# Kernel tuning notes

Measured on AMD Instinct MI355X. Metric: run time of the kernel, lower is better.

## Reference

```python
import jax, jax.numpy as jnp
import numpy as np

B, L, S, D = 32, 256, 4, 512
H = L * S  # history_capacity
TGB = 128
VOCAB = 50000
LN_EPS = 1e-5


def _layer_norm(x, gamma, beta):
    mu = jnp.mean(x, axis=-1, keepdims=True)
    var = jnp.var(x, axis=-1, keepdims=True)
    return (x - mu) * jax.lax.rsqrt(var + LN_EPS) * gamma + beta


def setup_inputs() -> dict:
    key = jax.random.key(0)
    ks = jax.random.split(key, 16)
    inp = {
        'embed_table': jax.random.normal(ks[0], (VOCAB, D), jnp.float32) * 0.02,
        'time_gap_emb': jax.random.normal(ks[1], (TGB + 1, D), jnp.float32) * 0.02,
        'seq_id_emb': jax.random.normal(ks[2], (S + 1, D), jnp.float32) * 0.02,
        'pos_emb': jax.random.normal(ks[3], (L, D), jnp.float32) * 0.02,
        'ln_gamma': jnp.ones((5 * D,), jnp.float32),
        'ln_beta': jnp.zeros((5 * D,), jnp.float32),
        'w1': jax.random.normal(ks[4], (5 * D, 4 * D), jnp.float32) * (1.0 / np.sqrt(5 * D)),
        'b1': jnp.zeros((4 * D,), jnp.float32),
        'w2': jax.random.normal(ks[5], (4 * D, D), jnp.float32) * (1.0 / np.sqrt(4 * D)),
        'b2': jnp.zeros((D,), jnp.float32),
        'empty_tokens': jax.random.normal(ks[6], (S, D), jnp.float32) * 0.02,
        'history_tokens': jax.random.randint(ks[7], (B, H), 0, VOCAB, jnp.int64 if jax.config.jax_enable_x64 else jnp.int32),
        'post_tokens': jax.random.randint(ks[8], (B, H), 0, VOCAB),
        'author_tokens': jax.random.randint(ks[9], (B, H), 0, VOCAB),
        'action_tokens': jax.random.randint(ks[10], (B, H), 0, VOCAB),
        'time_gap': jax.random.randint(ks[11], (B, H), 0, TGB + 1),
        'group_ids': jax.random.randint(ks[12], (B, H), 0, S + 1),
        'lengths': jax.random.randint(ks[13], (B,), 0, H + 1),
    }
    return inp


def reference(embed_table, time_gap_emb, seq_id_emb, pos_emb, ln_gamma, ln_beta,
              w1, b1, w2, b2, empty_tokens,
              history_tokens, post_tokens, author_tokens, action_tokens,
              time_gap, group_ids, lengths):
    # padded-dense validity mask: positions < lengths  [B,H]
    history_mask = jnp.arange(H)[None, :] < lengths[:, None]
    # zero out padded tokens (to_padded_dense pads with 0)
    hm_i = history_mask.astype(history_tokens.dtype)
    ht = history_tokens * hm_i
    pt = post_tokens * hm_i
    at = author_tokens * hm_i
    ct = action_tokens * hm_i
    tg = jnp.clip(time_gap * hm_i, 0, TGB)
    gid = group_ids * hm_i

    # event feature: 4 token embeds + time-gap embed -> [B,H,5D]
    event_inputs = jnp.concatenate(
        [embed_table[ht], embed_table[pt], embed_table[at], embed_table[ct],
         time_gap_emb[tg]], axis=-1)
    x = _layer_norm(event_inputs, ln_gamma, ln_beta)
    h = jax.nn.silu(x @ w1 + b1)          # dropout is eval-mode no-op
    event_tokens = h @ w2 + b2            # [B,H,D]

    # per-(batch, group) bucketization: keep last L valid positions of each group
    grp = jnp.arange(1, S + 1)
    mask_bs = history_mask[:, None, :] & (gid[:, None, :] == grp[None, :, None])  # [B,S,H]
    cum = jnp.cumsum(mask_bs.astype(jnp.int32), axis=-1)
    count = cum[..., -1]                                  # [B,S]
    offset = jnp.maximum(count - L, 0)                    # drop all but last L
    rank0 = cum - 1
    keep = mask_bs & (rank0 >= offset[..., None])
    dest = jnp.where(keep, rank0 - offset[..., None], L)  # slot L = dump slot

    def scatter_one(tokens, d):  # tokens [H,D], d [H] -> [L,D]
        return jnp.zeros((L + 1, D), tokens.dtype).at[d].set(tokens)[:L]

    # vmap over batch then group
    states = jax.vmap(lambda tok, ds: jax.vmap(lambda d: scatter_one(tok, d))(ds))(
        event_tokens, dest)                               # [B,S,L,D]

    # empty groups get the learned empty token at slot 0
    is_empty = (count == 0)                               # [B,S]
    slot0 = (jnp.arange(L) == 0)                          # [L]
    states = jnp.where((is_empty[:, :, None] & slot0[None, None, :])[..., None],
                       empty_tokens[None, :, None, :], states)
    kept = jnp.where(is_empty, 1, jnp.minimum(count, L))  # [B,S]
    sequence_mask = jnp.arange(L)[None, None, :] < kept[..., None]  # [B,S,L]

    states = states + pos_emb[None, None, :, :] + seq_id_emb[1:][None, :, None, :]
    states = states * sequence_mask[..., None].astype(states.dtype)
    return states, sequence_mask
```

## Files before the change

kernel.cpp:

```cpp
#include <hip/hip_runtime.h>
#include <hip/hip_bf16.h>
#include <stdint.h>

#define NB 32
#define NL 256
#define NS 4
#define ND 512
#define NH 1024
#define FIVE_D 2560
#define HID 2048
#define MMAX 32768

typedef __bf16 bf16_t;
typedef __bf16 bf16x4 __attribute__((ext_vector_type(4)));
typedef __bf16 bf16x8 __attribute__((ext_vector_type(8)));
typedef float f32x4 __attribute__((ext_vector_type(4)));

__device__ __forceinline__ void async_ld16(const void* g, void* l) {
  __builtin_amdgcn_global_load_lds(
      (__attribute__((address_space(1))) void*)(uintptr_t)g,
      (__attribute__((address_space(3))) void*)(uintptr_t)l, 16, 0, 0);
}

__global__ void build_index_kernel(const int* __restrict__ group_ids,
                                   const int* __restrict__ lengths,
                                   int* __restrict__ n_rows,
                                   int* __restrict__ row_src,
                                   int* __restrict__ row_dst,
                                   const float* __restrict__ empty_tokens,
                                   const float* __restrict__ pos_emb,
                                   const float* __restrict__ seq_emb,
                                   float* __restrict__ out,
                                   float* __restrict__ mask) {
  const int g = blockIdx.x;
  const int b = g >> 2, s = g & 3;
  const int t = threadIdx.x;
  const int lane = t & 63, w = t >> 6;
  int len = lengths[b];
  len = len < 0 ? 0 : (len > NH ? NH : len);
  const int* gi = group_ids + b * NH;

  __shared__ int wtot[16];
  __shared__ int sbase;

  bool valid[4];
#pragma unroll
  for (int c = 0; c < 4; ++c) {
    int h = c * 256 + t;
    valid[c] = (h < len) && (gi[h] == s + 1);
    unsigned long long m = __ballot(valid[c]);
    if (lane == 0) wtot[c * 4 + w] = __popcll(m);
  }
  __syncthreads();

  int pre[16];
  int run = 0;
#pragma unroll
  for (int i = 0; i < 16; ++i) { pre[i] = run; run += wtot[i]; }
  const int count = run;
  const int keff = count < NL ? count : NL;
  const int offset = count - keff;

  if (t == 0) sbase = atomicAdd(n_rows, keff);
  __syncthreads();
  const int base = sbase;

  const unsigned long long lt = (1ull << lane) - 1ull;
#pragma unroll
  for (int c = 0; c < 4; ++c) {
    unsigned long long m = __ballot(valid[c]);
    if (valid[c]) {
      int rank = pre[c * 4 + w] + __popcll(m & lt);
      if (rank >= offset) {
        int slot = rank - offset;
        row_src[base + slot] = b * NH + c * 256 + t;
        row_dst[base + slot] = g * NL + slot;
      }
    }
  }

  const bool empty = (count == 0);
  const int keptm = empty ? 1 : keff;
  mask[g * NL + t] = (t < keptm) ? 1.f : 0.f;

  float* basep = out + (size_t)g * NL * ND;
  if (empty) {
    for (int d = t; d < ND; d += 256)
      basep[d] = empty_tokens[s * ND + d] + pos_emb[d] +
                 seq_emb[(s + 1) * ND + d];
  }
  int start = empty ? 1 : keff;
  uint4* p = (uint4*)basep;
  uint4 z; z.x = z.y = z.z = z.w = 0u;
  for (int i = start * (ND / 4) + t; i < NL * (ND / 4); i += 256) p[i] = z;
}

template <int KD, int NDIM>
__global__ void transpose_cvt_kernel(const float* __restrict__ src,
                                     bf16_t* __restrict__ dst) {
  __shared__ float tile[32][33];
  int k0 = blockIdx.y * 32, n0 = blockIdx.x * 32;
  int tx = threadIdx.x & 31, ty = threadIdx.x >> 5;
#pragma unroll
  for (int i = 0; i < 32; i += 8)
    tile[ty + i][tx] = src[(size_t)(k0 + ty + i) * NDIM + n0 + tx];
  __syncthreads();
#pragma unroll
  for (int i = 0; i < 32; i += 8)
    dst[(size_t)(n0 + ty + i) * KD + k0 + tx] = (bf16_t)tile[tx][ty + i];
}

__launch_bounds__(128)
__global__ void gather_ln_kernel(const float* __restrict__ embed,
                                 const float* __restrict__ tg_emb,
                                 const int* __restrict__ ht,
                                 const int* __restrict__ pt,
                                 const int* __restrict__ at,
                                 const int* __restrict__ ct,
                                 const int* __restrict__ tg,
                                 const float* __restrict__ gamma,
                                 const float* __restrict__ beta,
                                 const int* __restrict__ n_rows,
                                 const int* __restrict__ row_src,
                                 int row_base, int chunk,
                                 bf16_t* __restrict__ X) {
  const int t = threadIdx.x;
  const int w = t >> 6;
  const int M = *n_rows;
  int lim = row_base + chunk;
  if (lim > M) lim = M;

  __shared__ float red2[2][4];
  int par = 0;

  const int o = t * 4;

  for (int r = row_base + blockIdx.x; r < lim; r += gridDim.x) {
    const int rl = r - row_base;
    const int pos = row_src[r];

    const float* s0 = embed + (size_t)ht[pos] * ND;
    const float* s1 = embed + (size_t)pt[pos] * ND;
    const float* s2 = embed + (size_t)at[pos] * ND;
    const float* s3 = embed + (size_t)ct[pos] * ND;
    int tgv = tg[pos];
    tgv = tgv < 0 ? 0 : (tgv > 128 ? 128 : tgv);
    const float* s4 = tg_emb + (size_t)tgv * ND;

    float4 v0 = *(const float4*)(s0 + o);
    float4 v1 = *(const float4*)(s1 + o);
    float4 v2 = *(const float4*)(s2 + o);
    float4 v3 = *(const float4*)(s3 + o);
    float4 v4 = *(const float4*)(s4 + o);

    float sum = v0.x + v0.y + v0.z + v0.w + v1.x + v1.y + v1.z + v1.w +
                v2.x + v2.y + v2.z + v2.w + v3.x + v3.y + v3.z + v3.w +
                v4.x + v4.y + v4.z + v4.w;
    float sq = v0.x * v0.x + v0.y * v0.y + v0.z * v0.z + v0.w * v0.w +
               v1.x * v1.x + v1.y * v1.y + v1.z * v1.z + v1.w * v1.w +
               v2.x * v2.x + v2.y * v2.y + v2.z * v2.z + v2.w * v2.w +
               v3.x * v3.x + v3.y * v3.y + v3.z * v3.z + v3.w * v3.w +
               v4.x * v4.x + v4.y * v4.y + v4.z * v4.z + v4.w * v4.w;
#pragma unroll
    for (int off = 32; off > 0; off >>= 1) {
      sum += __shfl_xor(sum, off);
      sq += __shfl_xor(sq, off);
    }
    if ((t & 63) == 0) { red2[par][w] = sum; red2[par][2 + w] = sq; }
    __syncthreads();
    const float S = red2[par][0] + red2[par][1];
    const float Q = red2[par][2] + red2[par][3];
    par ^= 1;
    const float mu = S * (1.f / FIVE_D);
    const float var = Q * (1.f / FIVE_D) - mu * mu;
    const float rstd = rsqrtf(var + 1e-5f);

    bf16_t* xr = X + (size_t)rl * FIVE_D;
#define LN_STORE(vk, kk)                                                     \
    do {                                                                     \
      float4 gm = *(const float4*)(gamma + (kk)*512 + o);                    \
      float4 bt = *(const float4*)(beta + (kk)*512 + o);                     \
      bf16x4 ov;                                                             \
      ov[0] = (bf16_t)((vk.x - mu) * rstd * gm.x + bt.x);                    \
      ov[1] = (bf16_t)((vk.y - mu) * rstd * gm.y + bt.y);                    \
      ov[2] = (bf16_t)((vk.z - mu) * rstd * gm.z + bt.z);                    \
      ov[3] = (bf16_t)((vk.w - mu) * rstd * gm.w + bt.w);                    \
      *(bf16x4*)(xr + (kk)*512 + o) = ov;                                    \
    } while (0)
    LN_STORE(v0, 0);
    LN_STORE(v1, 1);
    LN_STORE(v2, 2);
    LN_STORE(v3, 3);
    LN_STORE(v4, 4);
#undef LN_STORE
  }
}

#define FENCE asm volatile("" ::: "memory")
#define BARRIER do { FENCE; __builtin_amdgcn_s_barrier(); FENCE; } while (0)
#define WAIT_VM(n) asm volatile("s_waitcnt vmcnt(" #n ")" ::: "memory")

template <int KD, int LDC>
__launch_bounds__(512, 2)
__global__ void gemm256_kernel(const bf16_t* __restrict__ A,
                               const bf16_t* __restrict__ Bt,
                               const int* __restrict__ nrows_p,
                               int row_base,
                               const float* __restrict__ bias,
                               bf16_t* __restrict__ Cb) {
  static_assert(KD % 64 == 0 && KD / 64 >= 2, "KD");
  const int M = *nrows_p;
  const int m0 = blockIdx.x * 256;
  if (row_base + m0 >= M) return;
  const int n0 = blockIdx.y * 256;

  extern __shared__ char smem[];

  const int t = threadIdx.x;
  const int lane = t & 63;
  const int wv = t >> 6;
  const int wm = wv >> 2;
  const int wn = wv & 3;
  const int l15 = lane & 15;
  const int l4 = lane >> 4;

  const int r0 = t >> 3;
  const int sq = (t & 7) ^ (r0 & 7);
  const bf16_t* Ab = A + (size_t)(m0 + r0) * KD + sq * 8;
  const bf16_t* Bb = Bt + (size_t)(n0 + r0) * KD + sq * 8;
  const int dst16 = t * 16;

  const int cs0 = (l4 ^ (l15 & 7)) << 4;
  const int cs1 = cs0 ^ 64;
  const int arow = (wm * 128 + l15) * 128;
  const int brow = (wn * 64 + l15) * 128;

  f32x4 acc[2][2][4][2] = {};
  bf16x8 a[4][2], bl[2][2], bh[2][2];

#define STAGE_A(dbuf, h, kofs)                                               \
  do {                                                                       \
    char* _d = smem + (dbuf) * 65536 + (h) * 16384 + dst16;                  \
    async_ld16(Ab + (size_t)((h) * 128) * KD + (kofs), _d);                  \
    async_ld16(Ab + (size_t)((h) * 128 + 64) * KD + (kofs), _d + 8192);      \
  } while (0)
#define STAGE_B(dbuf, h, kofs)                                               \
  do {                                                                       \
    char* _d = smem + (dbuf) * 65536 + 32768 + (h) * 16384 + dst16;          \
    async_ld16(Bb + (size_t)((h) * 128) * KD + (kofs), _d);                  \
    async_ld16(Bb + (size_t)((h) * 128 + 64) * KD + (kofs), _d + 8192);      \
  } while (0)
#define LOAD_A(cbuf, mh)                                                     \
  do {                                                                       \
    const char* _s = smem + (cbuf) * 65536 + (mh) * 8192 + arow;             \
    _Pragma("unroll") for (int _i = 0; _i < 4; ++_i) {                       \
      a[_i][0] = *(const bf16x8*)(_s + _i * 2048 + cs0);                     \
      a[_i][1] = *(const bf16x8*)(_s + _i * 2048 + cs1);                     \
    }                                                                        \
  } while (0)
#define LOAD_B(dst, cbuf, nh)                                                \
  do {                                                                       \
    const char* _s = smem + (cbuf) * 65536 + 32768 + (nh) * 4096 + brow;     \
    _Pragma("unroll") for (int _j = 0; _j < 2; ++_j) {                       \
      dst[_j][0] = *(const bf16x8*)(_s + _j * 2048 + cs0);                   \
      dst[_j][1] = *(const bf16x8*)(_s + _j * 2048 + cs1);                   \
    }                                                                        \
  } while (0)
#define MMA(mh, nh, B)                                                       \
  do {                                                                       \
    _Pragma("unroll") for (int _i = 0; _i < 4; ++_i)                         \
    _Pragma("unroll") for (int _j = 0; _j < 2; ++_j) {                       \
      acc[mh][nh][_i][_j] = __builtin_amdgcn_mfma_f32_16x16x32_bf16(         \
          a[_i][0], B[_j][0], acc[mh][nh][_i][_j], 0, 0, 0);                 \
      acc[mh][nh][_i][_j] = __builtin_amdgcn_mfma_f32_16x16x32_bf16(         \
          a[_i][1], B[_j][1], acc[mh][nh][_i][_j], 0, 0, 0);                 \
    }                                                                        \
  } while (0)

  constexpr int NT = KD / 64;

  STAGE_A(0, 0, 0);
  STAGE_A(0, 1, 0);
  STAGE_B(0, 0, 0);
  STAGE_B(0, 1, 0);

  int c = 0;
  for (int tk = 1; tk < NT; ++tk) {
    const int kn = tk * 64;
    const int d = c ^ 1;
    STAGE_A(d, 0, kn);
    STAGE_A(d, 1, kn);
    WAIT_VM(4);
    BARRIER;
    LOAD_A(c, 0);
    LOAD_B(bl, c, 0);
    __builtin_amdgcn_s_setprio(1);
    MMA(0, 0, bl);
    __builtin_amdgcn_s_setprio(0);
    STAGE_B(d, 0, kn);
    STAGE_B(d, 1, kn);
    LOAD_B(bh, c, 1);
    __builtin_amdgcn_s_setprio(1);
    MMA(0, 1, bh);
    __builtin_amdgcn_s_setprio(0);
    LOAD_A(c, 1);
    __builtin_amdgcn_s_setprio(1);
    MMA(1, 1, bh);
    MMA(1, 0, bl);
    __builtin_amdgcn_s_setprio(0);
    BARRIER;
    c = d;
  }

  WAIT_VM(0);
  BARRIER;
  LOAD_A(c, 0);
  LOAD_B(bl, c, 0);
  MMA(0, 0, bl);
  LOAD_B(bh, c, 1);
  MMA(0, 1, bh);
  LOAD_A(c, 1);
  MMA(1, 1, bh);
  MMA(1, 0, bl);

#pragma unroll
  for (int mh = 0; mh < 2; ++mh)
#pragma unroll
    for (int i = 0; i < 4; ++i) {
      const int rbase = m0 + wm * 128 + mh * 64 + i * 16 + l4 * 4;
#pragma unroll
      for (int nh = 0; nh < 2; ++nh)
#pragma unroll
        for (int j = 0; j < 2; ++j) {
          const int n = n0 + wn * 64 + nh * 32 + j * 16 + l15;
          const float bn = bias[n];
#pragma unroll
          for (int q = 0; q < 4; ++q) {
            float v = acc[mh][nh][i][j][q] + bn;
            v = v / (1.f + __expf(-v));
            Cb[(size_t)(rbase + q) * LDC + n] = (bf16_t)v;
          }
        }
    }
#undef STAGE_A
#undef STAGE_B
#undef LOAD_A
#undef LOAD_B
#undef MMA
}

template <int KD>
__launch_bounds__(512, 2)
__global__ void gemm128_scatter_kernel(const bf16_t* __restrict__ A,
                                       const bf16_t* __restrict__ Bt,
                                       const int* __restrict__ nrows_p,
                                       int row_base,
                                       const float* __restrict__ bias,
                                       const int* __restrict__ row_dst,
                                       const float* __restrict__ pos_emb,
                                       const float* __restrict__ seq_emb,
                                       float* __restrict__ out) {
  static_assert(KD % 64 == 0 && KD / 64 >= 2, "KD");
  const int M = *nrows_p;
  const int m0 = blockIdx.x * 128;
  if (row_base + m0 >= M) return;
  const int n0 = blockIdx.y * 128;

  extern __shared__ char smem[];

  const int t = threadIdx.x;
  const int lane = t & 63;
  const int wv = t >> 6;
  const int wm = wv >> 1;
  const int wn = wv & 1;
  const int l15 = lane & 15;
  const int l4 = lane >> 4;

  const int r0 = t >> 3;
  const int sq = (t & 7) ^ (r0 & 7);
  const bf16_t* Ab = A + (size_t)(m0 + r0) * KD + sq * 8;
  const bf16_t* Bb = Bt + (size_t)(n0 + r0) * KD + sq * 8;
  const int dst16 = t * 16;

  const int cs0 = (l4 ^ (l15 & 7)) << 4;
  const int cs1 = cs0 ^ 64;
  const int arow = (wm * 32 + l15) * 128;
  const int brow = (wn * 64 + l15) * 128;

  f32x4 acc[2][4] = {};
  bf16x8 a[2][2], b[4][2];

#define STAGE_A2(dbuf, kofs)                                                 \
  do {                                                                       \
    char* _d = smem + (dbuf) * 32768 + dst16;                                \
    async_ld16(Ab + (kofs), _d);                                             \
    async_ld16(Ab + (size_t)64 * KD + (kofs), _d + 8192);                    \
  } while (0)
#define STAGE_B2(dbuf, kofs)                                                 \
  do {                                                                       \
    char* _d = smem + (dbuf) * 32768 + 16384 + dst16;                        \
    async_ld16(Bb + (kofs), _d);                                             \
    async_ld16(Bb + (size_t)64 * KD + (kofs), _d + 8192);                    \
  } while (0)
#define LOAD_A2(cbuf)                                                        \
  do {                                                                       \
    const char* _s = smem + (cbuf) * 32768 + arow;                           \
    _Pragma("unroll") for (int _i = 0; _i < 2; ++_i) {                       \
      a[_i][0] = *(const bf16x8*)(_s + _i * 2048 + cs0);                     \
      a[_i][1] = *(const bf16x8*)(_s + _i * 2048 + cs1);                     \
    }                                                                        \
  } while (0)
#define LOAD_B2(cbuf)                                                        \
  do {                                                                       \
    const char* _s = smem + (cbuf) * 32768 + 16384 + brow;                   \
    _Pragma("unroll") for (int _j = 0; _j < 4; ++_j) {                       \
      b[_j][0] = *(const bf16x8*)(_s + _j * 2048 + cs0);                     \
      b[_j][1] = *(const bf16x8*)(_s + _j * 2048 + cs1);                     \
    }                                                                        \
  } while (0)
#define MMA2                                                                 \
  do {                                                                       \
    _Pragma("unroll") for (int _i = 0; _i < 2; ++_i)                         \
    _Pragma("unroll") for (int _j = 0; _j < 4; ++_j) {                       \
      acc[_i][_j] = __builtin_amdgcn_mfma_f32_16x16x32_bf16(                 \
          a[_i][0], b[_j][0], acc[_i][_j], 0, 0, 0);                         \
      acc[_i][_j] = __builtin_amdgcn_mfma_f32_16x16x32_bf16(                 \
          a[_i][1], b[_j][1], acc[_i][_j], 0, 0, 0);                         \
    }                                                                        \
  } while (0)

  constexpr int NT = KD / 64;

  STAGE_A2(0, 0);
  STAGE_B2(0, 0);

  int c = 0;
  for (int tk = 1; tk < NT; ++tk) {
    const int kn = tk * 64;
    const int d = c ^ 1;
    STAGE_A2(d, kn);
    WAIT_VM(2);
    BARRIER;
    LOAD_A2(c);
    LOAD_B2(c);
    STAGE_B2(d, kn);
    __builtin_amdgcn_s_setprio(1);
    MMA2;
    __builtin_amdgcn_s_setprio(0);
    BARRIER;
    c = d;
  }

  WAIT_VM(0);
  BARRIER;
  LOAD_A2(c);
  LOAD_B2(c);
  MMA2;

#pragma unroll
  for (int i = 0; i < 2; ++i) {
    int mbase = m0 + wm * 32 + i * 16 + l4 * 4;
#pragma unroll
    for (int q = 0; q < 4; ++q) {
      int r = mbase + q;
      if (row_base + r >= M) continue;
      int dst = row_dst[row_base + r];
      int slot = dst & (NL - 1);
      int sg = (dst >> 8) & 3;
#pragma unroll
      for (int j = 0; j < 4; ++j) {
        int n = n0 + wn * 64 + j * 16 + l15;
        float v = acc[i][j][q] + bias[n] + pos_emb[slot * ND + n] +
                  seq_emb[(sg + 1) * ND + n];
        out[(size_t)dst * ND + n] = v;
      }
    }
  }
#undef STAGE_A2
#undef STAGE_B2
#undef LOAD_A2
#undef LOAD_B2
#undef MMA2
}

extern "C" void kernel_launch(void* const* d_in, const int* in_sizes, int n_in,
                              void* d_out, int out_size, void* d_ws,
                              size_t ws_size, hipStream_t stream) {
  const float* embed_table = (const float*)d_in[0];
  const float* time_gap_emb = (const float*)d_in[1];
  const float* seq_id_emb = (const float*)d_in[2];
  const float* pos_emb = (const float*)d_in[3];
  const float* ln_gamma = (const float*)d_in[4];
  const float* ln_beta = (const float*)d_in[5];
  const float* w1 = (const float*)d_in[6];
  const float* b1 = (const float*)d_in[7];
  const float* w2 = (const float*)d_in[8];
  const float* b2 = (const float*)d_in[9];
  const float* empty_tokens = (const float*)d_in[10];
  const int* history_tokens = (const int*)d_in[11];
  const int* post_tokens = (const int*)d_in[12];
  const int* author_tokens = (const int*)d_in[13];
  const int* action_tokens = (const int*)d_in[14];
  const int* time_gap = (const int*)d_in[15];
  const int* group_ids = (const int*)d_in[16];
  const int* lengths = (const int*)d_in[17];

  const size_t fixed = 266240 + (size_t)(HID * FIVE_D + ND * HID) * 2;
  int chunk, nchunk;
  if (ws_size >= fixed + (size_t)32768 * 9216) { chunk = 32768; nchunk = 1; }
  else if (ws_size >= fixed + (size_t)16384 * 9216) { chunk = 16384; nchunk = 2; }
  else { chunk = 8192; nchunk = 4; }

  char* ws = (char*)d_ws;
  int* n_rows = (int*)ws;
  int* row_src = (int*)(ws + 4096);
  int* row_dst = (int*)(ws + 4096 + 131072);
  bf16_t* W1T = (bf16_t*)(ws + 266240);
  bf16_t* W2T = W1T + (size_t)HID * FIVE_D;
  bf16_t* Xc = W2T + (size_t)ND * HID;
  bf16_t* H1c = Xc + (size_t)chunk * FIVE_D;

  float* out_states = (float*)d_out;
  float* out_mask = out_states + (size_t)NB * NS * NL * ND;

  (void)hipFuncSetAttribute(
      reinterpret_cast<const void*>(gemm256_kernel<FIVE_D, HID>),
      hipFuncAttributeMaxDynamicSharedMemorySize, 131072);
  (void)hipFuncSetAttribute(
      reinterpret_cast<const void*>(gemm128_scatter_kernel<HID>),
      hipFuncAttributeMaxDynamicSharedMemorySize, 65536);

  hipMemsetAsync(n_rows, 0, 4, stream);

  build_index_kernel<<<NB * NS, 256, 0, stream>>>(
      group_ids, lengths, n_rows, row_src, row_dst, empty_tokens, pos_emb,
      seq_id_emb, out_states, out_mask);

  transpose_cvt_kernel<FIVE_D, HID>
      <<<dim3(HID / 32, FIVE_D / 32), 256, 0, stream>>>(w1, W1T);
  transpose_cvt_kernel<HID, ND>
      <<<dim3(ND / 32, HID / 32), 256, 0, stream>>>(w2, W2T);

  for (int c = 0; c < nchunk; ++c) {
    int row_base = c * chunk;
    gather_ln_kernel<<<4096, 128, 0, stream>>>(
        embed_table, time_gap_emb, history_tokens, post_tokens, author_tokens,
        action_tokens, time_gap, ln_gamma, ln_beta, n_rows, row_src, row_base,
        chunk, Xc);

    gemm256_kernel<FIVE_D, HID>
        <<<dim3(chunk / 256, HID / 256), 512, 131072, stream>>>(
            Xc, W1T, n_rows, row_base, b1, H1c);

    gemm128_scatter_kernel<HID>
        <<<dim3(chunk / 128, ND / 128), 512, 65536, stream>>>(
            H1c, W2T, n_rows, row_base, b2, row_dst, pos_emb, seq_id_emb,
            out_states);
  }
}
```

Baseline: 401.0 us.

## Split build-index zeroing across four blocks; one wavefront per row in gather-LN

```diff
diff --git a/kernel.cpp b/kernel.cpp
--- a/kernel.cpp
+++ b/kernel.cpp
@@ -32,7 +32,8 @@
                                    const float* __restrict__ seq_emb,
                                    float* __restrict__ out,
                                    float* __restrict__ mask) {
-  const int g = blockIdx.x;
+  const int g = blockIdx.x >> 2;
+  const int qtr = blockIdx.x & 3;
   const int b = g >> 2, s = g & 3;
   const int t = threadIdx.x;
   const int lane = t & 63, w = t >> 6;
@@ -61,38 +62,46 @@
   const int keff = count < NL ? count : NL;
   const int offset = count - keff;
 
-  if (t == 0) sbase = atomicAdd(n_rows, keff);
-  __syncthreads();
-  const int base = sbase;
-
-  const unsigned long long lt = (1ull << lane) - 1ull;
-#pragma unroll
-  for (int c = 0; c < 4; ++c) {
-    unsigned long long m = __ballot(valid[c]);
-    if (valid[c]) {
-      int rank = pre[c * 4 + w] + __popcll(m & lt);
-      if (rank >= offset) {
-        int slot = rank - offset;
-        row_src[base + slot] = b * NH + c * 256 + t;
-        row_dst[base + slot] = g * NL + slot;
+  const bool empty = (count == 0);
+  const int start = empty ? 1 : keff;
+
+  if (qtr == 0) {
+    if (t == 0) sbase = atomicAdd(n_rows, keff);
+    __syncthreads();
+    const int base = sbase;
+
+    const unsigned long long lt = (1ull << lane) - 1ull;
+#pragma unroll
+    for (int c = 0; c < 4; ++c) {
+      unsigned long long m = __ballot(valid[c]);
+      if (valid[c]) {
+        int rank = pre[c * 4 + w] + __popcll(m & lt);
+        if (rank >= offset) {
+          int slot = rank - offset;
+          row_src[base + slot] = b * NH + c * 256 + t;
+          row_dst[base + slot] = g * NL + slot;
+        }
       }
     }
-  }
-
-  const bool empty = (count == 0);
-  const int keptm = empty ? 1 : keff;
-  mask[g * NL + t] = (t < keptm) ? 1.f : 0.f;
-
-  float* basep = out + (size_t)g * NL * ND;
-  if (empty) {
-    for (int d = t; d < ND; d += 256)
-      basep[d] = empty_tokens[s * ND + d] + pos_emb[d] +
-                 seq_emb[(s + 1) * ND + d];
-  }
-  int start = empty ? 1 : keff;
-  uint4* p = (uint4*)basep;
-  uint4 z; z.x = z.y = z.z = z.w = 0u;
-  for (int i = start * (ND / 4) + t; i < NL * (ND / 4); i += 256) p[i] = z;
+
+    const int keptm = empty ? 1 : keff;
+    mask[g * NL + t] = (t < keptm) ? 1.f : 0.f;
+
+    if (empty) {
+      float* basep = out + (size_t)g * NL * ND;
+      for (int d = t; d < ND; d += 256)
+        basep[d] = empty_tokens[s * ND + d] + pos_emb[d] +
+                   seq_emb[(s + 1) * ND + d];
+    }
+  }
+
+  int lo = qtr * 64; if (lo < start) lo = start;
+  const int hi = qtr * 64 + 64;
+  if (lo < hi) {
+    uint4* p = (uint4*)(out + (size_t)g * NL * ND);
+    uint4 z; z.x = z.y = z.z = z.w = 0u;
+    for (int i = lo * (ND / 4) + t; i < hi * (ND / 4); i += 256) p[i] = z;
+  }
 }
 
 template <int KD, int NDIM>
@@ -110,7 +119,7 @@
     dst[(size_t)(n0 + ty + i) * KD + k0 + tx] = (bf16_t)tile[tx][ty + i];
 }
 
-__launch_bounds__(128)
+__launch_bounds__(256)
 __global__ void gather_ln_kernel(const float* __restrict__ embed,
                                  const float* __restrict__ tg_emb,
                                  const int* __restrict__ ht,
@@ -124,18 +133,16 @@
                                  const int* __restrict__ row_src,
                                  int row_base, int chunk,
                                  bf16_t* __restrict__ X) {
-  const int t = threadIdx.x;
-  const int w = t >> 6;
+  const int l = threadIdx.x & 63;
+  const int wid = blockIdx.x * 4 + (threadIdx.x >> 6);
+  const int wstride = gridDim.x * 4;
   const int M = *n_rows;
   int lim = row_base + chunk;
   if (lim > M) lim = M;
 
-  __shared__ float red2[2][4];
-  int par = 0;
-
-  const int o = t * 4;
-
-  for (int r = row_base + blockIdx.x; r < lim; r += gridDim.x) {
+  const int o = l * 4;
+
+  for (int r = row_base + wid; r < lim; r += wstride) {
     const int rl = r - row_base;
     const int pos = row_src[r];
 
@@ -148,50 +155,51 @@
     const float* s4 = tg_emb + (size_t)tgv * ND;
 
     float4 v0 = *(const float4*)(s0 + o);
-    float4 v1 = *(const float4*)(s1 + o);
-    float4 v2 = *(const float4*)(s2 + o);
-    float4 v3 = *(const float4*)(s3 + o);
-    float4 v4 = *(const float4*)(s4 + o);
-
-    float sum = v0.x + v0.y + v0.z + v0.w + v1.x + v1.y + v1.z + v1.w +
-                v2.x + v2.y + v2.z + v2.w + v3.x + v3.y + v3.z + v3.w +
-                v4.x + v4.y + v4.z + v4.w;
-    float sq = v0.x * v0.x + v0.y * v0.y + v0.z * v0.z + v0.w * v0.w +
-               v1.x * v1.x + v1.y * v1.y + v1.z * v1.z + v1.w * v1.w +
-               v2.x * v2.x + v2.y * v2.y + v2.z * v2.z + v2.w * v2.w +
-               v3.x * v3.x + v3.y * v3.y + v3.z * v3.z + v3.w * v3.w +
-               v4.x * v4.x + v4.y * v4.y + v4.z * v4.z + v4.w * v4.w;
+    float4 v1 = *(const float4*)(s0 + 256 + o);
+    float4 v2 = *(const float4*)(s1 + o);
+    float4 v3 = *(const float4*)(s1 + 256 + o);
+    float4 v4 = *(const float4*)(s2 + o);
+    float4 v5 = *(const float4*)(s2 + 256 + o);
+    float4 v6 = *(const float4*)(s3 + o);
+    float4 v7 = *(const float4*)(s3 + 256 + o);
+    float4 v8 = *(const float4*)(s4 + o);
+    float4 v9 = *(const float4*)(s4 + 256 + o);
+
+    float sum = 0.f, sq = 0.f;
+#define ACC(vk)                                                              \
+    do {                                                                     \
+      sum += vk.x + vk.y + vk.z + vk.w;                                      \
+      sq += vk.x * vk.x + vk.y * vk.y + vk.z * vk.z + vk.w * vk.w;           \
+    } while (0)
+    ACC(v0); ACC(v1); ACC(v2); ACC(v3); ACC(v4);
+    ACC(v5); ACC(v6); ACC(v7); ACC(v8); ACC(v9);
+#undef ACC
 #pragma unroll
     for (int off = 32; off > 0; off >>= 1) {
       sum += __shfl_xor(sum, off);
       sq += __shfl_xor(sq, off);
     }
-    if ((t & 63) == 0) { red2[par][w] = sum; red2[par][2 + w] = sq; }
-    __syncthreads();
-    const float S = red2[par][0] + red2[par][1];
-    const float Q = red2[par][2] + red2[par][3];
-    par ^= 1;
-    const float mu = S * (1.f / FIVE_D);
-    const float var = Q * (1.f / FIVE_D) - mu * mu;
+    const float mu = sum * (1.f / FIVE_D);
+    const float var = sq * (1.f / FIVE_D) - mu * mu;
     const float rstd = rsqrtf(var + 1e-5f);
 
     bf16_t* xr = X + (size_t)rl * FIVE_D;
-#define LN_STORE(vk, kk)                                                     \
+#define LN_STORE(vk, kofs)                                                   \
     do {                                                                     \
-      float4 gm = *(const float4*)(gamma + (kk)*512 + o);                    \
-      float4 bt = *(const float4*)(beta + (kk)*512 + o);                     \
+      float4 gm = *(const float4*)(gamma + (kofs) + o);                      \
+      float4 bt = *(const float4*)(beta + (kofs) + o);                       \
       bf16x4 ov;                                                             \
       ov[0] = (bf16_t)((vk.x - mu) * rstd * gm.x + bt.x);                    \
       ov[1] = (bf16_t)((vk.y - mu) * rstd * gm.y + bt.y);                    \
       ov[2] = (bf16_t)((vk.z - mu) * rstd * gm.z + bt.z);                    \
       ov[3] = (bf16_t)((vk.w - mu) * rstd * gm.w + bt.w);                    \
-      *(bf16x4*)(xr + (kk)*512 + o) = ov;                                    \
+      *(bf16x4*)(xr + (kofs) + o) = ov;                                      \
     } while (0)
-    LN_STORE(v0, 0);
-    LN_STORE(v1, 1);
-    LN_STORE(v2, 2);
-    LN_STORE(v3, 3);
-    LN_STORE(v4, 4);
+    LN_STORE(v0, 0);    LN_STORE(v1, 256);
+    LN_STORE(v2, 512);  LN_STORE(v3, 768);
+    LN_STORE(v4, 1024); LN_STORE(v5, 1280);
+    LN_STORE(v6, 1536); LN_STORE(v7, 1792);
+    LN_STORE(v8, 2048); LN_STORE(v9, 2304);
 #undef LN_STORE
   }
 }
@@ -532,7 +540,7 @@
 
   hipMemsetAsync(n_rows, 0, 4, stream);
 
-  build_index_kernel<<<NB * NS, 256, 0, stream>>>(
+  build_index_kernel<<<NB * NS * 4, 256, 0, stream>>>(
       group_ids, lengths, n_rows, row_src, row_dst, empty_tokens, pos_emb,
       seq_id_emb, out_states, out_mask);
 
@@ -543,7 +551,7 @@
 
   for (int c = 0; c < nchunk; ++c) {
     int row_base = c * chunk;
-    gather_ln_kernel<<<4096, 128, 0, stream>>>(
+    gather_ln_kernel<<<2048, 256, 0, stream>>>(
         embed_table, time_gap_emb, history_tokens, post_tokens, author_tokens,
         action_tokens, time_gap, ln_gamma, ln_beta, n_rows, row_src, row_base,
         chunk, Xc);
```

Result: no change. 395.8 us (-1.3%).
